# Optimization experiments

Measured on AMD Instinct MI355X. Metric: run time of the kernel, lower is better.

The kernel has to match this reference:

```python
import jax, jax.numpy as jnp
import numpy as np

N_NODES = 100000
N_HYPEREDGES = 20000
NNZ = 600000
D = 128


def setup_inputs() -> dict:
    key = jax.random.key(0)
    k = jax.random.split(key, 6)
    s = 1.0 / np.sqrt(D)
    x = jax.random.normal(k[0], (N_NODES, D), jnp.float32)
    node_idx = jax.random.randint(k[1], (NNZ,), 0, N_NODES, dtype=jnp.int64 if jax.config.jax_enable_x64 else jnp.int32)
    edge_idx = jax.random.randint(k[2], (NNZ,), 0, N_HYPEREDGES, dtype=jnp.int64 if jax.config.jax_enable_x64 else jnp.int32)
    conv_W = jax.random.uniform(k[3], (D, D), jnp.float32, -s, s)
    conv_b = jnp.zeros((D,), jnp.float32)
    res_W = jax.random.uniform(k[4], (D, D), jnp.float32, -s, s)
    res_b = jax.random.uniform(k[5], (D,), jnp.float32, -s, s)
    return {"x": x, "node_idx": node_idx, "edge_idx": edge_idx,
            "conv_W": conv_W, "conv_b": conv_b, "res_W": res_W, "res_b": res_b}


def hypergraph_conv(x, node_idx, edge_idx, W, b):
    # PyG HypergraphConv (no attention, unit hyperedge weights):
    #   out = D^{-1} H B^{-1} H^T (x W) + b
    y = x @ W                                                      # [N, D]
    ones = jnp.ones(node_idx.shape, dtype=y.dtype)
    deg_n = jax.ops.segment_sum(ones, node_idx, num_segments=N_NODES)        # node degree
    deg_e = jax.ops.segment_sum(ones, edge_idx, num_segments=N_HYPEREDGES)   # hyperedge size
    inv_n = jnp.where(deg_n > 0, 1.0 / deg_n, 0.0)
    inv_e = jnp.where(deg_e > 0, 1.0 / deg_e, 0.0)
    # node -> hyperedge aggregation, normalized by B^{-1}
    e_feat = jax.ops.segment_sum(y[node_idx], edge_idx, num_segments=N_HYPEREDGES)
    e_feat = e_feat * inv_e[:, None]                               # [E, D]
    # hyperedge -> node aggregation, normalized by D^{-1}
    out = jax.ops.segment_sum(e_feat[edge_idx], node_idx, num_segments=N_NODES)
    out = out * inv_n[:, None]                                     # [N, D]
    return out + b


def reference(x, node_idx, edge_idx, conv_W, conv_b, res_W, res_b):
    h = hypergraph_conv(x, node_idx, edge_idx, conv_W, conv_b)     # layer_num = 1
    return (x @ res_W + res_b) + h                                 # residual Linear + conv out
```

## Files before the change

### kernel.cpp

```cpp
#include <hip/hip_runtime.h>

#define N_NODES 100000
#define N_EDGES 20000
#define NNZ_C   600000
#define D 128

typedef short bf16x8 __attribute__((ext_vector_type(8)));
typedef float f32x4  __attribute__((ext_vector_type(4)));

__device__ __forceinline__ unsigned short f2bf(float f) {
    unsigned int u = __float_as_uint(f);
    u = (u + 0x7fffu + ((u >> 16) & 1u)) >> 16;
    return (unsigned short)u;
}
__device__ __forceinline__ float bf2f(unsigned short h) {
    return __uint_as_float((unsigned int)h << 16);
}
__device__ __forceinline__ unsigned int pk_trunc(float lo, float hi) {
    return __builtin_amdgcn_perm(__float_as_uint(hi), __float_as_uint(lo),
                                 0x07060302);
}

#define CHA 8192
#define NBLK_A 74
#define EBW 32
#define NBE 625
#define ECAP 1536
#define NBW 32
#define NBN 3125
#define NCAP 512

__global__ __launch_bounds__(256) void bin_pass(
    const int* __restrict__ nidx, const int* __restrict__ eidx,
    const float* __restrict__ cW, const float* __restrict__ rW,
    unsigned short* __restrict__ wtc, unsigned short* __restrict__ wtr,
    int* __restrict__ bucket_e, int* __restrict__ bucket_n,
    int* __restrict__ gcur_e, int* __restrict__ gcur_n) {
    const int bid = blockIdx.x;
    if (bid >= NBLK_A) {
        const int t0 = (bid - NBLK_A) * 4096;
        for (int i = threadIdx.x; i < 4096; i += 256) {
            const int t = t0 + i;
            const int m = t >> 14, idx = t & 16383;
            const int f = idx & 127, k = idx >> 7;
            const float* src = m ? rW : cW;
            unsigned short* dst = m ? wtr : wtc;
            dst[f * D + k] = f2bf(src[k * D + f]);
        }
        return;
    }
    const int jbeg = bid * CHA;
    const int jend = (jbeg + CHA < NNZ_C) ? jbeg + CHA : NNZ_C;
    __shared__ int cnt_e[NBE], base_e[NBE];
    __shared__ int cnt_n[NBN], base_n[NBN];
    for (int i = threadIdx.x; i < NBE; i += 256) cnt_e[i] = 0;
    for (int i = threadIdx.x; i < NBN; i += 256) cnt_n[i] = 0;
    __syncthreads();
    for (int j = jbeg + threadIdx.x; j < jend; j += 256) {
        atomicAdd(&cnt_e[eidx[j] >> 5], 1);
        atomicAdd(&cnt_n[nidx[j] >> 5], 1);
    }
    __syncthreads();
    for (int i = threadIdx.x; i < NBE; i += 256) {
        const int c = cnt_e[i];
        base_e[i] = c ? atomicAdd(&gcur_e[i], c) : 0;
        cnt_e[i] = 0;
    }
    for (int i = threadIdx.x; i < NBN; i += 256) {
        const int c = cnt_n[i];
        base_n[i] = c ? atomicAdd(&gcur_n[i], c) : 0;
        cnt_n[i] = 0;
    }
    __syncthreads();
    for (int j = jbeg + threadIdx.x; j < jend; j += 256) {
        const int e = eidx[j], n = nidx[j];
        {
            const int b = e >> 5;
            const int pos = base_e[b] + atomicAdd(&cnt_e[b], 1);
            if (pos < ECAP) bucket_e[b * ECAP + pos] = ((e & 31) << 17) | n;
        }
        {
            const int b = n >> 5;
            const int pos = base_n[b] + atomicAdd(&cnt_n[b], 1);
            if (pos < NCAP) bucket_n[b * NCAP + pos] = ((n & 31) << 15) | e;
        }
    }
}

#define GT 64
#define XPAD 136
#define NTILES ((N_NODES + GT - 1) / GT)

__device__ __forceinline__ void stage_tile(unsigned short* __restrict__ buf,
                                           const float* __restrict__ x,
                                           int tile, int r0, int qp) {
    int n = tile * GT + r0;
    if (n >= N_NODES) n = N_NODES - 1;
    const float* xr = x + (size_t)n * D + qp * 16;
    unsigned short* dst = buf + r0 * XPAD + qp * 16;
#pragma unroll
    for (int u = 0; u < 2; ++u) {
        const float4 a = *(const float4*)(xr + u * 8);
        const float4 c = *(const float4*)(xr + u * 8 + 4);
        uint4 v;
        v.x = pk_trunc(a.x, a.y);
        v.y = pk_trunc(a.z, a.w);
        v.z = pk_trunc(c.x, c.y);
        v.w = pk_trunc(c.z, c.w);
        *(uint4*)(dst + u * 8) = v;
    }
}

__device__ __forceinline__ void compute_tile(
    const unsigned short* __restrict__ buf, const bf16x8 (&A)[2][4],
    int tile, int mat, int fh, int quad, int l16,
    unsigned short* __restrict__ yb, unsigned short* __restrict__ resb) {
    f32x4 acc[4][2] = {};
#pragma unroll
    for (int g = 0; g < 4; ++g)
#pragma unroll
        for (int kc = 0; kc < 4; ++kc) {
            const bf16x8 B = *(const bf16x8*)(buf + (g * 16 + l16) * XPAD +
                                              kc * 32 + quad * 8);
            acc[g][0] = __builtin_amdgcn_mfma_f32_16x16x32_bf16(A[0][kc], B, acc[g][0], 0, 0, 0);
            acc[g][1] = __builtin_amdgcn_mfma_f32_16x16x32_bf16(A[1][kc], B, acc[g][1], 0, 0, 0);
        }
    const int nbase = tile * GT;
    unsigned short* dst = mat ? resb : yb;
#pragma unroll
    for (int g = 0; g < 4; ++g) {
        const int n = nbase + g * 16 + l16;
        if (n >= N_NODES) continue;
#pragma unroll
        for (int ft = 0; ft < 2; ++ft) {
            const int f0 = fh + ft * 16 + quad * 4;
            uint2 v;
            v.x = pk_trunc(acc[g][ft][0], acc[g][ft][1]);
            v.y = pk_trunc(acc[g][ft][2], acc[g][ft][3]);
            *(uint2*)(dst + (size_t)n * D + f0) = v;
        }
    }
}

__global__ __launch_bounds__(512) void mfma_gemm(
    const float* __restrict__ x, const unsigned short* __restrict__ wtc,
    const unsigned short* __restrict__ wtr,
    unsigned short* __restrict__ yb, unsigned short* __restrict__ resb) {
    __shared__ unsigned short xs[2][GT * XPAD];

    const int w    = threadIdx.x >> 6;
    const int lane = threadIdx.x & 63;
    const int quad = lane >> 4;
    const int l16  = lane & 15;
    const int mat  = w & 1;
    const int fh   = (w >> 1) * 32;

    const unsigned short* wsrc = mat ? wtr : wtc;
    bf16x8 A[2][4];
#pragma unroll
    for (int ft = 0; ft < 2; ++ft)
#pragma unroll
        for (int kc = 0; kc < 4; ++kc)
            A[ft][kc] = *(const bf16x8*)(wsrc + (fh + ft * 16 + l16) * D +
                                         kc * 32 + quad * 8);

    const int r0 = threadIdx.x >> 3;
    const int qp = threadIdx.x & 7;
    const int t0 = blockIdx.x * 2;

    stage_tile(xs[0], x, t0, r0, qp);
    __syncthreads();
    stage_tile(xs[1], x, t0 + 1, r0, qp);
    compute_tile(xs[0], A, t0, mat, fh, quad, l16, yb, resb);
    __syncthreads();
    compute_tile(xs[1], A, t0 + 1, mat, fh, quad, l16, yb, resb);
}

__global__ __launch_bounds__(256) void edge_aggregate(
    const int* __restrict__ bucket_e, const int* __restrict__ gcur_e,
    const unsigned short* __restrict__ yb, unsigned short* __restrict__ efb) {
    __shared__ int raw[ECAP];
    __shared__ int srt[ECAP];
    __shared__ int cnt[EBW + 1];
    __shared__ int cur[EBW];
    const int tid = threadIdx.x;
    const int b = blockIdx.x;
    int W = gcur_e[b];
    if (W > ECAP) W = ECAP;
    if (tid < EBW + 1) cnt[tid] = 0;
    __syncthreads();
    const int* src = bucket_e + b * ECAP;
    for (int i = tid; i < W; i += 256) {
        const int p = src[i];
        raw[i] = p;
        atomicAdd(&cnt[p >> 17], 1);
    }
    __syncthreads();
    if (tid < EBW) {
        const int c = cnt[tid];
        int v = c;
#pragma unroll
        for (int off = 1; off < EBW; off <<= 1) {
            const int t = __shfl_up(v, off);
            if (tid >= off) v += t;
        }
        cnt[tid] = v - c;
        cur[tid] = v - c;
        if (tid == EBW - 1) cnt[EBW] = v;
    }
    __syncthreads();
    for (int i = tid; i < W; i += 256) {
        const int p = raw[i];
        const int pos = atomicAdd(&cur[p >> 17], 1);
        srt[pos] = p & 0x1FFFF;
    }
    __syncthreads();

    const int g = tid >> 4;
    const int l = tid & 15;
#pragma unroll
    for (int u = 0; u < 2; ++u) {
        const int el = g * 2 + u;
        const int beg = cnt[el], end = cnt[el + 1];
        float acc[8] = {};
        int j = beg;
        for (; j + 4 <= end; j += 4) {
            const int n0 = srt[j], n1 = srt[j + 1];
            const int n2 = srt[j + 2], n3 = srt[j + 3];
            const bf16x8 p0 = *(const bf16x8*)(yb + (size_t)n0 * D + l * 8);
            const bf16x8 p1 = *(const bf16x8*)(yb + (size_t)n1 * D + l * 8);
            const bf16x8 p2 = *(const bf16x8*)(yb + (size_t)n2 * D + l * 8);
            const bf16x8 p3 = *(const bf16x8*)(yb + (size_t)n3 * D + l * 8);
#pragma unroll
            for (int i = 0; i < 8; ++i)
                acc[i] += (bf2f((unsigned short)p0[i]) + bf2f((unsigned short)p1[i]))
                        + (bf2f((unsigned short)p2[i]) + bf2f((unsigned short)p3[i]));
        }
        for (; j < end; ++j) {
            const bf16x8 p = *(const bf16x8*)(yb + (size_t)srt[j] * D + l * 8);
#pragma unroll
            for (int i = 0; i < 8; ++i) acc[i] += bf2f((unsigned short)p[i]);
        }
        const int deg = end - beg;
        const float inv = deg ? 1.f / (float)deg : 0.f;
        bf16x8 o;
#pragma unroll
        for (int i = 0; i < 8; ++i) o[i] = (short)f2bf(acc[i] * inv);
        *(bf16x8*)(efb + (size_t)(b * EBW + el) * D + l * 8) = o;
    }
}

__global__ __launch_bounds__(256) void node_aggregate(
    const int* __restrict__ bucket_n, const int* __restrict__ gcur_n,
    const unsigned short* __restrict__ efb, const unsigned short* __restrict__ resb,
    const float* __restrict__ rb, const float* __restrict__ cb,
    float* __restrict__ out) {
    __shared__ int raw[NCAP];
    __shared__ int srt[NCAP];
    __shared__ int cnt[NBW + 1];
    __shared__ int cur[NBW];
    const int tid = threadIdx.x;
    const int b = blockIdx.x;
    int W = gcur_n[b];
    if (W > NCAP) W = NCAP;
    if (tid < NBW + 1) cnt[tid] = 0;
    __syncthreads();
    const int* src = bucket_n + b * NCAP;
    for (int i = tid; i < W; i += 256) {
        const int p = src[i];
        raw[i] = p;
        atomicAdd(&cnt[p >> 15], 1);
    }
    __syncthreads();
    if (tid < NBW) {
        const int c = cnt[tid];
        int v = c;
#pragma unroll
        for (int off = 1; off < NBW; off <<= 1) {
            const int t = __shfl_up(v, off);
            if (tid >= off) v += t;
        }
        cnt[tid] = v - c;
        cur[tid] = v - c;
        if (tid == NBW - 1) cnt[NBW] = v;
    }
    __syncthreads();
    for (int i = tid; i < W; i += 256) {
        const int p = raw[i];
        const int pos = atomicAdd(&cur[p >> 15], 1);
        srt[pos] = p & 0x7FFF;
    }
    __syncthreads();

    const int g = tid >> 4;
    const int l = tid & 15;
#pragma unroll
    for (int u = 0; u < 2; ++u) {
        const int nl = g * 2 + u;
        const int n = b * NBW + nl;
        const int beg = cnt[nl], end = cnt[nl + 1];
        float acc[8] = {};
        int j = beg;
        for (; j + 2 <= end; j += 2) {
            const int e0 = srt[j], e1 = srt[j + 1];
            const bf16x8 p0 = *(const bf16x8*)(efb + (size_t)e0 * D + l * 8);
            const bf16x8 p1 = *(const bf16x8*)(efb + (size_t)e1 * D + l * 8);
#pragma unroll
            for (int i = 0; i < 8; ++i)
                acc[i] += bf2f((unsigned short)p0[i]) + bf2f((unsigned short)p1[i]);
        }
        if (j < end) {
            const bf16x8 p = *(const bf16x8*)(efb + (size_t)srt[j] * D + l * 8);
#pragma unroll
            for (int i = 0; i < 8; ++i) acc[i] += bf2f((unsigned short)p[i]);
        }
        const int deg = end - beg;
        const float inv = deg ? 1.f / (float)deg : 0.f;
        const bf16x8 r = *(const bf16x8*)(resb + (size_t)n * D + l * 8);
        const float4 rb0 = *(const float4*)(rb + l * 8);
        const float4 rb1 = *(const float4*)(rb + l * 8 + 4);
        const float4 cb0 = *(const float4*)(cb + l * 8);
        const float4 cb1 = *(const float4*)(cb + l * 8 + 4);
        float4 o0, o1;
        o0.x = bf2f((unsigned short)r[0]) + acc[0] * inv + rb0.x + cb0.x;
        o0.y = bf2f((unsigned short)r[1]) + acc[1] * inv + rb0.y + cb0.y;
        o0.z = bf2f((unsigned short)r[2]) + acc[2] * inv + rb0.z + cb0.z;
        o0.w = bf2f((unsigned short)r[3]) + acc[3] * inv + rb0.w + cb0.w;
        o1.x = bf2f((unsigned short)r[4]) + acc[4] * inv + rb1.x + cb1.x;
        o1.y = bf2f((unsigned short)r[5]) + acc[5] * inv + rb1.y + cb1.y;
        o1.z = bf2f((unsigned short)r[6]) + acc[6] * inv + rb1.z + cb1.z;
        o1.w = bf2f((unsigned short)r[7]) + acc[7] * inv + rb1.w + cb1.w;
        const size_t o = (size_t)n * D + l * 8;
        *(float4*)(out + o) = o0;
        *(float4*)(out + o + 4) = o1;
    }
}

extern "C" void kernel_launch(void* const* d_in, const int* in_sizes, int n_in,
                              void* d_out, int out_size, void* d_ws,
                              size_t ws_size, hipStream_t stream) {
    const float* x  = (const float*)d_in[0];
    const int* nidx = (const int*)d_in[1];
    const int* eidx = (const int*)d_in[2];
    const float* cW = (const float*)d_in[3];
    const float* cb = (const float*)d_in[4];
    const float* rW = (const float*)d_in[5];
    const float* rb = (const float*)d_in[6];
    float* out = (float*)d_out;

    char* ws = (char*)d_ws;
    size_t off = 0;
    auto alloc = [&](size_t bytes) {
        size_t o = off;
        off += (bytes + 255) & ~(size_t)255;
        return o;
    };
    unsigned short* yb   = (unsigned short*)(ws + alloc((size_t)N_NODES * D * 2));
    unsigned short* resb = (unsigned short*)(ws + alloc((size_t)N_NODES * D * 2));
    unsigned short* efb  = (unsigned short*)(ws + alloc((size_t)N_EDGES * D * 2));
    unsigned short* wtc  = (unsigned short*)(ws + alloc((size_t)D * D * 2));
    unsigned short* wtr  = (unsigned short*)(ws + alloc((size_t)D * D * 2));
    int* bucket_e = (int*)(ws + alloc((size_t)NBE * ECAP * 4));
    int* bucket_n = (int*)(ws + alloc((size_t)NBN * NCAP * 4));
    int* gcur     = (int*)(ws + alloc((size_t)(NBE + NBN) * 4));
    int* gcur_e = gcur;
    int* gcur_n = gcur + NBE;

    hipMemsetAsync(gcur, 0, (size_t)(NBE + NBN) * 4, stream);

    bin_pass<<<NBLK_A + 8, 256, 0, stream>>>(nidx, eidx, cW, rW, wtc, wtr,
                                             bucket_e, bucket_n, gcur_e, gcur_n);

    mfma_gemm<<<(NTILES + 1) / 2, 512, 0, stream>>>(x, wtc, wtr, yb, resb);

    edge_aggregate<<<NBE, 256, 0, stream>>>(bucket_e, gcur_e, yb, efb);
    node_aggregate<<<NBN, 256, 0, stream>>>(bucket_n, gcur_n, efb, resb,
                                            rb, cb, out);
}
```

Before: 220.1 us.

## Replace block-local histogram binning with per-element global atomics

The binning pass no longer builds shared-memory histograms per 8192-element chunk and reserves ranges with one global atomic per bin. Each thread now handles one nonzero and does a global atomicAdd on the bucket cursor directly, with many more blocks launched. This removes the shared-memory counting passes and block barriers and raises parallelism. In exchange it adds 1.2M global atomics with contention on the 625 edge bins.

```diff
diff --git a/kernel.cpp b/kernel.cpp
--- a/kernel.cpp
+++ b/kernel.cpp
@@ -21,8 +21,7 @@
                                  0x07060302);
 }
 
-#define CHA 8192
-#define NBLK_A 74
+#define NBLK_A 2344
 #define EBW 32
 #define NBE 625
 #define ECAP 1536
@@ -49,41 +48,18 @@
         }
         return;
     }
-    const int jbeg = bid * CHA;
-    const int jend = (jbeg + CHA < NNZ_C) ? jbeg + CHA : NNZ_C;
-    __shared__ int cnt_e[NBE], base_e[NBE];
-    __shared__ int cnt_n[NBN], base_n[NBN];
-    for (int i = threadIdx.x; i < NBE; i += 256) cnt_e[i] = 0;
-    for (int i = threadIdx.x; i < NBN; i += 256) cnt_n[i] = 0;
-    __syncthreads();
-    for (int j = jbeg + threadIdx.x; j < jend; j += 256) {
-        atomicAdd(&cnt_e[eidx[j] >> 5], 1);
-        atomicAdd(&cnt_n[nidx[j] >> 5], 1);
-    }
-    __syncthreads();
-    for (int i = threadIdx.x; i < NBE; i += 256) {
-        const int c = cnt_e[i];
-        base_e[i] = c ? atomicAdd(&gcur_e[i], c) : 0;
-        cnt_e[i] = 0;
-    }
-    for (int i = threadIdx.x; i < NBN; i += 256) {
-        const int c = cnt_n[i];
-        base_n[i] = c ? atomicAdd(&gcur_n[i], c) : 0;
-        cnt_n[i] = 0;
-    }
-    __syncthreads();
-    for (int j = jbeg + threadIdx.x; j < jend; j += 256) {
-        const int e = eidx[j], n = nidx[j];
-        {
-            const int b = e >> 5;
-            const int pos = base_e[b] + atomicAdd(&cnt_e[b], 1);
-            if (pos < ECAP) bucket_e[b * ECAP + pos] = ((e & 31) << 17) | n;
-        }
-        {
-            const int b = n >> 5;
-            const int pos = base_n[b] + atomicAdd(&cnt_n[b], 1);
-            if (pos < NCAP) bucket_n[b * NCAP + pos] = ((n & 31) << 15) | e;
-        }
+    const int j = bid * 256 + threadIdx.x;
+    if (j >= NNZ_C) return;
+    const int e = eidx[j], n = nidx[j];
+    {
+        const int b = e >> 5;
+        const int pos = atomicAdd(&gcur_e[b], 1);
+        if (pos < ECAP) bucket_e[b * ECAP + pos] = ((e & 31) << 17) | n;
+    }
+    {
+        const int b = n >> 5;
+        const int pos = atomicAdd(&gcur_n[b], 1);
+        if (pos < NCAP) bucket_n[b * NCAP + pos] = ((n & 31) << 15) | e;
     }
 }
 
```

After: 347.3 us. +57.8%, slower.
